# Kernel optimization log

Measured on AMD Instinct MI355X. Metric: run time of the kernel, lower is better.

Reference implementation:

```python
import jax, jax.numpy as jnp
import numpy as np
from jax import lax

B = 8192      # number of independent rods (batch)
N = 128       # vertices per rod; N-1 = 127 sequential edge constraints
TOL = 1e-6    # early-exit tolerance from the original solver


def setup_inputs() -> dict:
    key = jax.random.key(0)
    k1, k2, k3, k4, k5 = jax.random.split(key, 5)
    current_vertices = jax.random.normal(k1, (B, N, 3), dtype=jnp.float32)
    # strictly positive nominal segment lengths
    nominal_length = jax.random.uniform(k2, (B, N - 1), dtype=jnp.float32) + 0.1
    # scale is a divisor -> keep it bounded away from zero
    scale = jax.random.uniform(k3, (2 * B, N - 1), dtype=jnp.float32) + 0.5
    mass_scale = jax.random.normal(k4, (2 * B, N - 1, 3, 3), dtype=jnp.float32) * 0.1
    # float 0/1 mask (mostly ones, a few frozen edges)
    zero_mask_num = (jax.random.uniform(k5, (B, N - 1)) > 0.05).astype(jnp.float32)
    return {
        "current_vertices": current_vertices,
        "nominal_length": nominal_length,
        "scale": scale,
        "mass_scale": mass_scale,
        "zero_mask_num": zero_mask_num,
    }


def _solve(current_vertices, nominal_length, scale, mass_scale, zero_mask_num):
    Bb, Nn, _ = current_vertices.shape
    E = Nn - 1
    # per-edge quantities, laid out with the (sequential) edge axis leading
    nl_sq = (nominal_length * nominal_length).T                     # (E, B)
    # rows of scale/mass_scale are interleaved as s_idx = 2*b + v
    sc = scale.reshape(Bb, 2, E).transpose(2, 0, 1)                 # (E, B, 2)
    ms = mass_scale.reshape(Bb, 2, E, 3, 3).transpose(2, 0, 1, 3, 4)  # (E, B, 2, 3, 3)
    zm = zero_mask_num.T                                            # (E, B)
    idx = jnp.arange(E)

    def step(verts, xs):
        i, nlsq_i, sc_i, ms_i, zm_i = xs
        vv = lax.dynamic_slice_in_dim(verts, i, 2, axis=1)          # (B, 2, 3)
        edges = (vv[:, 1] - vv[:, 0]) * zm_i[:, None]               # (B, 3)
        denom = nlsq_i + jnp.sum(edges * edges, axis=-1)            # (B,)
        l = jnp.where(zm_i != 0.0, 1.0 - 2.0 * nlsq_i / denom, 0.0)  # (B,)
        all_small = jnp.all(jnp.abs(l) < TOL)                       # early-exit condition
        # (mass_scale * l/scale) @ edges for both endpoints of the edge
        result = jnp.einsum('bvrc,bv,bc->bvr', ms_i, l[:, None] / sc_i, edges)  # (B, 2, 3)
        upd = jnp.where(all_small, 0.0, result)
        verts = lax.dynamic_update_slice_in_dim(verts, vv + upd, i, axis=1)
        return verts, None

    out, _ = lax.scan(step, current_vertices, (idx, nl_sq, sc, ms, zm))
    return out


def reference(current_vertices, nominal_length, scale, mass_scale, zero_mask_num):
    return _solve(current_vertices, nominal_length, scale, mass_scale, zero_mask_num)
```

## Files before the change

kernel.cpp:

```cpp
#include <hip/hip_runtime.h>

#define BATCH 8192
#define NV 128
#define NE 127
#define NCHUNK 31

struct Buf {
  float ms0[36];
  float ms1[36];
  float v[12];
  float nl[4];
  float zm[4];
  float s0[4];
  float s1[4];
};

__device__ __forceinline__ void load_chunk(Buf& B, int c,
    const float* __restrict__ vin, const float* __restrict__ nl,
    const float* __restrict__ zm, const float* __restrict__ sc0,
    const float* __restrict__ sc1, const float* __restrict__ ms0,
    const float* __restrict__ ms1) {
  const float* m0 = ms0 + 36 * c;
  const float* m1 = ms1 + 36 * c;
#pragma unroll
  for (int i = 0; i < 36; ++i) B.ms0[i] = m0[i];
#pragma unroll
  for (int i = 0; i < 36; ++i) B.ms1[i] = m1[i];
  const float* vp = vin + 12 * c + 3;
#pragma unroll
  for (int i = 0; i < 12; ++i) B.v[i] = vp[i];
#pragma unroll
  for (int i = 0; i < 4; ++i) B.nl[i] = nl[4 * c + i];
#pragma unroll
  for (int i = 0; i < 4; ++i) B.zm[i] = zm[4 * c + i];
#pragma unroll
  for (int i = 0; i < 4; ++i) B.s0[i] = sc0[4 * c + i];
#pragma unroll
  for (int i = 0; i < 4; ++i) B.s1[i] = sc1[4 * c + i];
}

__device__ __forceinline__ void compute_chunk(const Buf& B, int c,
    float& px, float& py, float& pz, float* __restrict__ vout) {
#pragma unroll
  for (int k = 0; k < 4; ++k) {
    const int e4 = 4 * c + k;
    float qx = B.v[3 * k + 0], qy = B.v[3 * k + 1], qz = B.v[3 * k + 2];
    float zmv = B.zm[k];
    float ex = (qx - px) * zmv;
    float ey = (qy - py) * zmv;
    float ez = (qz - pz) * zmv;
    float nlv = B.nl[k];
    float nlsq = nlv * nlv;
    float denom = nlsq + (ex * ex + ey * ey + ez * ez);
    float l = 1.0f - 2.0f * nlsq * __builtin_amdgcn_rcpf(denom);
    float f0 = l * __builtin_amdgcn_rcpf(B.s0[k]);
    float f1 = l * __builtin_amdgcn_rcpf(B.s1[k]);
    float u0x = (B.ms0[9*k+0] * ex + B.ms0[9*k+1] * ey + B.ms0[9*k+2] * ez) * f0;
    float u0y = (B.ms0[9*k+3] * ex + B.ms0[9*k+4] * ey + B.ms0[9*k+5] * ez) * f0;
    float u0z = (B.ms0[9*k+6] * ex + B.ms0[9*k+7] * ey + B.ms0[9*k+8] * ez) * f0;
    float u1x = (B.ms1[9*k+0] * ex + B.ms1[9*k+1] * ey + B.ms1[9*k+2] * ez) * f1;
    float u1y = (B.ms1[9*k+3] * ex + B.ms1[9*k+4] * ey + B.ms1[9*k+5] * ez) * f1;
    float u1z = (B.ms1[9*k+6] * ex + B.ms1[9*k+7] * ey + B.ms1[9*k+8] * ez) * f1;
    vout[3 * e4 + 0] = px + u0x;
    vout[3 * e4 + 1] = py + u0y;
    vout[3 * e4 + 2] = pz + u0z;
    px = qx + u1x;
    py = qy + u1y;
    pz = qz + u1z;
  }
}

__global__ __launch_bounds__(32, 1) void rod_kernel(
    const float* __restrict__ vin_g,
    const float* __restrict__ nl_g,
    const float* __restrict__ sc_g,
    const float* __restrict__ ms_g,
    const float* __restrict__ zm_g,
    float* __restrict__ vout_g) {
  int b = blockIdx.x * blockDim.x + threadIdx.x;
  if (b >= BATCH) return;

  const float* __restrict__ vin  = vin_g  + (size_t)b * (NV * 3);
  float* __restrict__       vout = vout_g + (size_t)b * (NV * 3);
  const float* __restrict__ nl  = nl_g + (size_t)b * NE;
  const float* __restrict__ zm  = zm_g + (size_t)b * NE;
  const float* __restrict__ sc0 = sc_g + (size_t)(2 * b) * NE;
  const float* __restrict__ sc1 = sc0 + NE;
  const float* __restrict__ ms0 = ms_g + (size_t)(2 * b) * NE * 9;
  const float* __restrict__ ms1 = ms0 + (size_t)NE * 9;

  float px = vin[0], py = vin[1], pz = vin[2];

  Buf B0, B1, B2;
  load_chunk(B0, 0, vin, nl, zm, sc0, sc1, ms0, ms1);
  load_chunk(B1, 1, vin, nl, zm, sc0, sc1, ms0, ms1);
  load_chunk(B2, 2, vin, nl, zm, sc0, sc1, ms0, ms1);

  int c = 0;
  for (int t = 0; t < 10; ++t, c += 3) {
    compute_chunk(B0, c + 0, px, py, pz, vout);
    if (c + 3 < NCHUNK) load_chunk(B0, c + 3, vin, nl, zm, sc0, sc1, ms0, ms1);
    compute_chunk(B1, c + 1, px, py, pz, vout);
    if (c + 4 < NCHUNK) load_chunk(B1, c + 4, vin, nl, zm, sc0, sc1, ms0, ms1);
    compute_chunk(B2, c + 2, px, py, pz, vout);
    if (c + 5 < NCHUNK) load_chunk(B2, c + 5, vin, nl, zm, sc0, sc1, ms0, ms1);
  }
  compute_chunk(B0, 30, px, py, pz, vout);

  for (int e = 124; e < NE; ++e) {
    float qx = vin[3 * e + 3];
    float qy = vin[3 * e + 4];
    float qz = vin[3 * e + 5];
    float zmv = zm[e];
    float ex = (qx - px) * zmv;
    float ey = (qy - py) * zmv;
    float ez = (qz - pz) * zmv;
    float nlv = nl[e];
    float nlsq = nlv * nlv;
    float denom = nlsq + (ex * ex + ey * ey + ez * ez);
    float l = 1.0f - 2.0f * nlsq * __builtin_amdgcn_rcpf(denom);
    float f0 = l * __builtin_amdgcn_rcpf(sc0[e]);
    float f1 = l * __builtin_amdgcn_rcpf(sc1[e]);
    const float* m0 = ms0 + 9 * e;
    const float* m1 = ms1 + 9 * e;
    float u0x = (m0[0] * ex + m0[1] * ey + m0[2] * ez) * f0;
    float u0y = (m0[3] * ex + m0[4] * ey + m0[5] * ez) * f0;
    float u0z = (m0[6] * ex + m0[7] * ey + m0[8] * ez) * f0;
    float u1x = (m1[0] * ex + m1[1] * ey + m1[2] * ez) * f1;
    float u1y = (m1[3] * ex + m1[4] * ey + m1[5] * ez) * f1;
    float u1z = (m1[6] * ex + m1[7] * ey + m1[8] * ez) * f1;
    vout[3 * e + 0] = px + u0x;
    vout[3 * e + 1] = py + u0y;
    vout[3 * e + 2] = pz + u0z;
    px = qx + u1x;
    py = qy + u1y;
    pz = qz + u1z;
  }
  vout[3 * NE + 0] = px;
  vout[3 * NE + 1] = py;
  vout[3 * NE + 2] = pz;
}

extern "C" void kernel_launch(void* const* d_in, const int* in_sizes, int n_in,
                              void* d_out, int out_size, void* d_ws, size_t ws_size,
                              hipStream_t stream) {
  const float* vin = (const float*)d_in[0];
  const float* nl  = (const float*)d_in[1];
  const float* sc  = (const float*)d_in[2];
  const float* ms  = (const float*)d_in[3];
  const float* zm  = (const float*)d_in[4];
  float* vout = (float*)d_out;

  dim3 grid(BATCH / 32);
  dim3 block(32);
  hipLaunchKernelGGL(rod_kernel, grid, block, 0, stream, vin, nl, sc, ms, zm, vout);
}
```

Baseline: 163.7 us.

## Use 8-byte vector loads/stores with aligned offsets and shrink blocks to 8 threads

Loads of mass_scale, vertices and scale are re-expressed as float2 vector loads, using pointers shifted by one element so every access is 8-byte aligned, and outputs for each 4-edge chunk are buffered and written as float2 stores. This cuts the number of memory instructions per thread. Blocks also shrink from 32 to 8 threads, spreading the 8192 rods over 1024 workgroups so more CUs are used. The cost is wider register buffers and partially filled wavefronts, which waste SIMD lanes.

```diff
diff --git a/kernel.cpp b/kernel.cpp
--- a/kernel.cpp
+++ b/kernel.cpp
@@ -5,46 +5,52 @@
 #define NE 127
 #define NCHUNK 31
 
+typedef float v2f __attribute__((ext_vector_type(2)));
+
 struct Buf {
-  float ms0[36];
-  float ms1[36];
-  float v[12];
+  v2f ms0[18];
+  v2f ms1w[19];
+  v2f vw[7];
+  v2f s0v[2];
+  v2f s1w[3];
   float nl[4];
   float zm[4];
-  float s0[4];
-  float s1[4];
 };
+
+#define MS0(k,j) (B.ms0[(9*(k)+(j))>>1][(9*(k)+(j))&1])
+#define MS1(k,j) (B.ms1w[(9*(k)+(j)+1)>>1][(9*(k)+(j)+1)&1])
+#define VV(j)    (B.vw[((j)+1)>>1][((j)+1)&1])
+#define S0k(k)   (B.s0v[(k)>>1][(k)&1])
+#define S1k(k)   (B.s1w[((k)+1)>>1][((k)+1)&1])
 
 __device__ __forceinline__ void load_chunk(Buf& B, int c,
     const float* __restrict__ vin, const float* __restrict__ nl,
     const float* __restrict__ zm, const float* __restrict__ sc0,
-    const float* __restrict__ sc1, const float* __restrict__ ms0,
-    const float* __restrict__ ms1) {
-  const float* m0 = ms0 + 36 * c;
-  const float* m1 = ms1 + 36 * c;
+    const float* __restrict__ sc1m1, const float* __restrict__ ms0,
+    const float* __restrict__ ms1m1) {
+  const v2f* __restrict__ pm0 = (const v2f*)(ms0 + 36 * c);
+  const v2f* __restrict__ pm1 = (const v2f*)(ms1m1 + 36 * c);
+  const v2f* __restrict__ pv  = (const v2f*)(vin + 12 * c + 2);
+  const v2f* __restrict__ ps0 = (const v2f*)(sc0 + 4 * c);
+  const v2f* __restrict__ ps1 = (const v2f*)(sc1m1 + 4 * c);
 #pragma unroll
-  for (int i = 0; i < 36; ++i) B.ms0[i] = m0[i];
+  for (int i = 0; i < 18; ++i) B.ms0[i] = pm0[i];
 #pragma unroll
-  for (int i = 0; i < 36; ++i) B.ms1[i] = m1[i];
-  const float* vp = vin + 12 * c + 3;
+  for (int i = 0; i < 19; ++i) B.ms1w[i] = pm1[i];
 #pragma unroll
-  for (int i = 0; i < 12; ++i) B.v[i] = vp[i];
+  for (int i = 0; i < 7; ++i) B.vw[i] = pv[i];
+  B.s0v[0] = ps0[0]; B.s0v[1] = ps0[1];
+  B.s1w[0] = ps1[0]; B.s1w[1] = ps1[1]; B.s1w[2] = ps1[2];
 #pragma unroll
-  for (int i = 0; i < 4; ++i) B.nl[i] = nl[4 * c + i];
-#pragma unroll
-  for (int i = 0; i < 4; ++i) B.zm[i] = zm[4 * c + i];
-#pragma unroll
-  for (int i = 0; i < 4; ++i) B.s0[i] = sc0[4 * c + i];
-#pragma unroll
-  for (int i = 0; i < 4; ++i) B.s1[i] = sc1[4 * c + i];
+  for (int i = 0; i < 4; ++i) { B.nl[i] = nl[4 * c + i]; B.zm[i] = zm[4 * c + i]; }
 }
 
 __device__ __forceinline__ void compute_chunk(const Buf& B, int c,
     float& px, float& py, float& pz, float* __restrict__ vout) {
+  float out[12];
 #pragma unroll
   for (int k = 0; k < 4; ++k) {
-    const int e4 = 4 * c + k;
-    float qx = B.v[3 * k + 0], qy = B.v[3 * k + 1], qz = B.v[3 * k + 2];
+    float qx = VV(3 * k + 0), qy = VV(3 * k + 1), qz = VV(3 * k + 2);
     float zmv = B.zm[k];
     float ex = (qx - px) * zmv;
     float ey = (qy - py) * zmv;
@@ -53,24 +59,27 @@
     float nlsq = nlv * nlv;
     float denom = nlsq + (ex * ex + ey * ey + ez * ez);
     float l = 1.0f - 2.0f * nlsq * __builtin_amdgcn_rcpf(denom);
-    float f0 = l * __builtin_amdgcn_rcpf(B.s0[k]);
-    float f1 = l * __builtin_amdgcn_rcpf(B.s1[k]);
-    float u0x = (B.ms0[9*k+0] * ex + B.ms0[9*k+1] * ey + B.ms0[9*k+2] * ez) * f0;
-    float u0y = (B.ms0[9*k+3] * ex + B.ms0[9*k+4] * ey + B.ms0[9*k+5] * ez) * f0;
-    float u0z = (B.ms0[9*k+6] * ex + B.ms0[9*k+7] * ey + B.ms0[9*k+8] * ez) * f0;
-    float u1x = (B.ms1[9*k+0] * ex + B.ms1[9*k+1] * ey + B.ms1[9*k+2] * ez) * f1;
-    float u1y = (B.ms1[9*k+3] * ex + B.ms1[9*k+4] * ey + B.ms1[9*k+5] * ez) * f1;
-    float u1z = (B.ms1[9*k+6] * ex + B.ms1[9*k+7] * ey + B.ms1[9*k+8] * ez) * f1;
-    vout[3 * e4 + 0] = px + u0x;
-    vout[3 * e4 + 1] = py + u0y;
-    vout[3 * e4 + 2] = pz + u0z;
+    float f0 = l * __builtin_amdgcn_rcpf(S0k(k));
+    float f1 = l * __builtin_amdgcn_rcpf(S1k(k));
+    float u0x = (MS0(k,0) * ex + MS0(k,1) * ey + MS0(k,2) * ez) * f0;
+    float u0y = (MS0(k,3) * ex + MS0(k,4) * ey + MS0(k,5) * ez) * f0;
+    float u0z = (MS0(k,6) * ex + MS0(k,7) * ey + MS0(k,8) * ez) * f0;
+    float u1x = (MS1(k,0) * ex + MS1(k,1) * ey + MS1(k,2) * ez) * f1;
+    float u1y = (MS1(k,3) * ex + MS1(k,4) * ey + MS1(k,5) * ez) * f1;
+    float u1z = (MS1(k,6) * ex + MS1(k,7) * ey + MS1(k,8) * ez) * f1;
+    out[3 * k + 0] = px + u0x;
+    out[3 * k + 1] = py + u0y;
+    out[3 * k + 2] = pz + u0z;
     px = qx + u1x;
     py = qy + u1y;
     pz = qz + u1z;
   }
+  v2f* __restrict__ po = (v2f*)(vout + 12 * c);
+#pragma unroll
+  for (int i = 0; i < 6; ++i) { v2f t; t.x = out[2*i]; t.y = out[2*i+1]; po[i] = t; }
 }
 
-__global__ __launch_bounds__(32, 1) void rod_kernel(
+__global__ __launch_bounds__(8, 1) void rod_kernel(
     const float* __restrict__ vin_g,
     const float* __restrict__ nl_g,
     const float* __restrict__ sc_g,
@@ -85,25 +94,25 @@
   const float* __restrict__ nl  = nl_g + (size_t)b * NE;
   const float* __restrict__ zm  = zm_g + (size_t)b * NE;
   const float* __restrict__ sc0 = sc_g + (size_t)(2 * b) * NE;
-  const float* __restrict__ sc1 = sc0 + NE;
+  const float* __restrict__ sc1m1 = sc0 + NE - 1;
   const float* __restrict__ ms0 = ms_g + (size_t)(2 * b) * NE * 9;
-  const float* __restrict__ ms1 = ms0 + (size_t)NE * 9;
+  const float* __restrict__ ms1m1 = ms0 + (size_t)NE * 9 - 1;
 
   float px = vin[0], py = vin[1], pz = vin[2];
 
   Buf B0, B1, B2;
-  load_chunk(B0, 0, vin, nl, zm, sc0, sc1, ms0, ms1);
-  load_chunk(B1, 1, vin, nl, zm, sc0, sc1, ms0, ms1);
-  load_chunk(B2, 2, vin, nl, zm, sc0, sc1, ms0, ms1);
+  load_chunk(B0, 0, vin, nl, zm, sc0, sc1m1, ms0, ms1m1);
+  load_chunk(B1, 1, vin, nl, zm, sc0, sc1m1, ms0, ms1m1);
+  load_chunk(B2, 2, vin, nl, zm, sc0, sc1m1, ms0, ms1m1);
 
   int c = 0;
   for (int t = 0; t < 10; ++t, c += 3) {
     compute_chunk(B0, c + 0, px, py, pz, vout);
-    if (c + 3 < NCHUNK) load_chunk(B0, c + 3, vin, nl, zm, sc0, sc1, ms0, ms1);
+    if (c + 3 < NCHUNK) load_chunk(B0, c + 3, vin, nl, zm, sc0, sc1m1, ms0, ms1m1);
     compute_chunk(B1, c + 1, px, py, pz, vout);
-    if (c + 4 < NCHUNK) load_chunk(B1, c + 4, vin, nl, zm, sc0, sc1, ms0, ms1);
+    if (c + 4 < NCHUNK) load_chunk(B1, c + 4, vin, nl, zm, sc0, sc1m1, ms0, ms1m1);
     compute_chunk(B2, c + 2, px, py, pz, vout);
-    if (c + 5 < NCHUNK) load_chunk(B2, c + 5, vin, nl, zm, sc0, sc1, ms0, ms1);
+    if (c + 5 < NCHUNK) load_chunk(B2, c + 5, vin, nl, zm, sc0, sc1m1, ms0, ms1m1);
   }
   compute_chunk(B0, 30, px, py, pz, vout);
 
@@ -120,9 +129,9 @@
     float denom = nlsq + (ex * ex + ey * ey + ez * ez);
     float l = 1.0f - 2.0f * nlsq * __builtin_amdgcn_rcpf(denom);
     float f0 = l * __builtin_amdgcn_rcpf(sc0[e]);
-    float f1 = l * __builtin_amdgcn_rcpf(sc1[e]);
+    float f1 = l * __builtin_amdgcn_rcpf(*(sc1m1 + 1 + e));
     const float* m0 = ms0 + 9 * e;
-    const float* m1 = ms1 + 9 * e;
+    const float* m1 = ms1m1 + 1 + 9 * e;
     float u0x = (m0[0] * ex + m0[1] * ey + m0[2] * ez) * f0;
     float u0y = (m0[3] * ex + m0[4] * ey + m0[5] * ez) * f0;
     float u0z = (m0[6] * ex + m0[7] * ey + m0[8] * ez) * f0;
@@ -151,7 +160,7 @@
   const float* zm  = (const float*)d_in[4];
   float* vout = (float*)d_out;
 
-  dim3 grid(BATCH / 32);
-  dim3 block(32);
+  dim3 grid(BATCH / 8);
+  dim3 block(8);
   hipLaunchKernelGGL(rod_kernel, grid, block, 0, stream, vin, nl, sc, ms, zm, vout);
 }
```

After: 180.7 us. 1.1x slower.
